# Optimization experiments

Measured on AMD Instinct MI355X. Metric: run time of the kernel, lower is better.

## Reference

```python
import jax, jax.numpy as jnp
import numpy as np

N_NODES = 4096
N_EDGES = 16384
L = 512
MP_STEPS = 5
DT = 0.01


def _mlp(x, W1, b1, W2, b2):
    return jax.nn.relu(x @ W1 + b1) @ W2 + b2


def _ln(x):
    m = jnp.mean(x, axis=-1, keepdims=True)
    v = jnp.var(x, axis=-1, keepdims=True)
    return (x - m) * jax.lax.rsqrt(v + 1e-6)


_PARAM_SHAPES = [
    ("enc_e_W1", (1, L)), ("enc_e_b1", (L,)), ("enc_e_W2", (L, L)), ("enc_e_b2", (L,)),
    ("enc_n_W1", (1, L)), ("enc_n_b1", (L,)), ("enc_n_W2", (L, L)), ("enc_n_b2", (L,)),
    ("proc_e_W1", (3 * L, L)), ("proc_e_b1", (L,)), ("proc_e_W2", (L, L)), ("proc_e_b2", (L,)),
    ("proc_n_W1", (2 * L, L)), ("proc_n_b1", (L,)), ("proc_n_W2", (L, L)), ("proc_n_b2", (L,)),
    ("dec_e_W1", (L, L)), ("dec_e_b1", (L,)), ("dec_e_W2", (L, 1)), ("dec_e_b2", (1,)),
]


def setup_inputs() -> dict:
    key = jax.random.key(0)
    ks = jax.random.split(key, 3 + len(_PARAM_SHAPES))
    d = {}
    d["state"] = jax.random.normal(ks[0], (N_EDGES + N_NODES,), dtype=jnp.float32)
    d["senders"] = jax.random.randint(ks[1], (N_EDGES,), 0, N_NODES)
    d["receivers"] = jax.random.randint(ks[2], (N_EDGES,), 0, N_NODES)
    for i, (name, shp) in enumerate(_PARAM_SHAPES):
        if name.endswith(("b1", "b2")):
            d[name] = jnp.zeros(shp, dtype=jnp.float32)
        else:
            d[name] = 0.02 * jax.random.normal(ks[3 + i], shp, dtype=jnp.float32)
    return d


def _hamiltonian(x, senders, receivers,
                 enc_e_W1, enc_e_b1, enc_e_W2, enc_e_b2,
                 enc_n_W1, enc_n_b1, enc_n_W2, enc_n_b2,
                 proc_e_W1, proc_e_b1, proc_e_W2, proc_e_b2,
                 proc_n_W1, proc_n_b1, proc_n_W2, proc_n_b2,
                 dec_e_W1, dec_e_b1, dec_e_W2, dec_e_b2):
    # graph_from_state: edge scalars then node scalars
    e = x[:N_EDGES].reshape(N_EDGES, 1)
    n = x[N_EDGES:].reshape(N_NODES, 1)
    # encode (MLP + layer norm)
    eh = _ln(_mlp(e, enc_e_W1, enc_e_b1, enc_e_W2, enc_e_b2))  # [E, L]
    nh = _ln(_mlp(n, enc_n_W1, enc_n_b1, enc_n_W2, enc_n_b2))  # [N, L]
    # process: num_mp_steps of GraphNetwork-style message passing, shared params
    for _ in range(MP_STEPS):
        msg_in = jnp.concatenate([eh, nh[senders], nh[receivers]], axis=-1)  # [E, 3L]
        eh = eh + _mlp(msg_in, proc_e_W1, proc_e_b1, proc_e_W2, proc_e_b2)
        agg = jax.ops.segment_sum(eh, receivers, num_segments=N_NODES)  # [N, L]
        node_in = jnp.concatenate([nh, agg], axis=-1)  # [N, 2L]
        nh = nh + _mlp(node_in, proc_n_W1, proc_n_b1, proc_n_W2, proc_n_b2)
    # decode edges to scalars; H = sum of decoded edge energies
    dec_e = _mlp(eh, dec_e_W1, dec_e_b1, dec_e_W2, dec_e_b2)  # [E, 1]
    return jnp.sum(dec_e)


def reference(state, senders, receivers,
              enc_e_W1, enc_e_b1, enc_e_W2, enc_e_b2,
              enc_n_W1, enc_n_b1, enc_n_W2, enc_n_b2,
              proc_e_W1, proc_e_b1, proc_e_W2, proc_e_b2,
              proc_n_W1, proc_n_b1, proc_n_W2, proc_n_b2,
              dec_e_W1, dec_e_b1, dec_e_W2, dec_e_b2):
    def H_fn(x):
        return _hamiltonian(x, senders, receivers,
                            enc_e_W1, enc_e_b1, enc_e_W2, enc_e_b2,
                            enc_n_W1, enc_n_b1, enc_n_W2, enc_n_b2,
                            proc_e_W1, proc_e_b1, proc_e_W2, proc_e_b2,
                            proc_n_W1, proc_n_b1, proc_n_W2, proc_n_b2,
                            dec_e_W1, dec_e_b1, dec_e_W2, dec_e_b2)
    H, dH = jax.value_and_grad(H_fn)(state)
    # one integrator step driven by the Hamiltonian gradient (stand-in for DAE solve)
    next_state = state - DT * dH
    return next_state
```

## Files before the change

kernel.cpp:

```cpp
#include <hip/hip_runtime.h>


#define E_ROWS 16384
#define N_ROWS 4096
#define DT_F   0.01f

typedef unsigned char u8;
typedef unsigned short u16;
typedef __attribute__((ext_vector_type(8))) short short8v;
typedef __attribute__((ext_vector_type(4))) float f32x4;

__device__ __forceinline__ u16 f2b(float f) {
    union { float f; unsigned u; } v; v.f = f;
    unsigned r = v.u + 0x7FFF + ((v.u >> 16) & 1);
    return (u16)(r >> 16);
}
__device__ __forceinline__ float b2f(u16 u) {
    union { unsigned u; float f; } v; v.u = ((unsigned)u) << 16;
    return v.f;
}

template<int KTOT, int LDA, int LDC, bool ADD_C, bool GATHER2, bool BIAS,
         bool RELU_MASK, bool APPLY_MASK, bool WF32, bool WBF16, bool DUALOUT>
__global__ __launch_bounds__(256)
void bgemm(const u16* __restrict__ A, const u16* __restrict__ Bt,
           float* __restrict__ C, u16* __restrict__ Cb,
           const float* __restrict__ Cin, const float* __restrict__ bias,
           const float* __restrict__ G12v,
           const int* __restrict__ sidx, const int* __restrict__ ridx,
           u8* __restrict__ maskw, float* __restrict__ C2)
{
    __shared__ u16 Al[4096];
    __shared__ u16 Bl[4096];
    const int tid = threadIdx.x;
    const int lane = tid & 63;
    const int wv = tid >> 6;
    const int wr = wv >> 1, wc = wv & 1;
    const int rowBase = blockIdx.y << 7;
    const int colBase = blockIdx.x << 7;

    const int srow = tid >> 2;
    const int kel = (tid & 3) << 3;
    const u16* Ag = A + (size_t)(rowBase + srow) * LDA + kel;
    const u16* Bg = Bt + (size_t)(colBase + srow) * KTOT + kel;
    u16* Ad = Al + (wv << 9);
    u16* Bd = Bl + (wv << 9);

    f32x4 acc[4][4];
#pragma unroll
    for (int i = 0; i < 4; ++i)
#pragma unroll
        for (int j = 0; j < 4; ++j)
            acc[i][j] = (f32x4){0.f, 0.f, 0.f, 0.f};

    const int arow = (wr << 6) + (lane & 15);
    const int brow = (wc << 6) + (lane & 15);
    const int koff = (lane >> 4) << 3;

    for (int kb = 0; kb < KTOT; kb += 32) {
        __builtin_amdgcn_global_load_lds((const __attribute__((address_space(1))) void*)(Ag + kb),
                                         (__attribute__((address_space(3))) void*)Ad, 16, 0, 0);
        __builtin_amdgcn_global_load_lds((const __attribute__((address_space(1))) void*)(Ag + kb + (size_t)64 * LDA),
                                         (__attribute__((address_space(3))) void*)(Ad + 2048), 16, 0, 0);
        __builtin_amdgcn_global_load_lds((const __attribute__((address_space(1))) void*)(Bg + kb),
                                         (__attribute__((address_space(3))) void*)Bd, 16, 0, 0);
        __builtin_amdgcn_global_load_lds((const __attribute__((address_space(1))) void*)(Bg + kb + (size_t)64 * KTOT),
                                         (__attribute__((address_space(3))) void*)(Bd + 2048), 16, 0, 0);
        __syncthreads();
        short8v af[4], bf[4];
#pragma unroll
        for (int i = 0; i < 4; ++i)
            af[i] = *(const short8v*)&Al[((arow + (i << 4)) << 5) + koff];
#pragma unroll
        for (int j = 0; j < 4; ++j)
            bf[j] = *(const short8v*)&Bl[((brow + (j << 4)) << 5) + koff];
#pragma unroll
        for (int i = 0; i < 4; ++i)
#pragma unroll
            for (int j = 0; j < 4; ++j)
                acc[i][j] = __builtin_amdgcn_mfma_f32_16x16x32_bf16(af[i], bf[j], acc[i][j], 0, 0, 0);
        __syncthreads();
    }

    const int colB = colBase + (wc << 6) + (lane & 15);
    const int rowB = rowBase + (wr << 6) + ((lane >> 4) << 2);
    float bcol[4];
    if (BIAS) {
#pragma unroll
        for (int j = 0; j < 4; ++j) bcol[j] = bias[colB + (j << 4)];
    }
    const bool upper = DUALOUT && (colBase >= 512);
#pragma unroll
    for (int i = 0; i < 4; ++i) {
#pragma unroll
        for (int r = 0; r < 4; ++r) {
            const int row = rowB + (i << 4) + r;
            int si = 0, ri = 0;
            if (GATHER2) { si = sidx[row]; ri = ridx[row]; }
#pragma unroll
            for (int j = 0; j < 4; ++j) {
                const int col = colB + (j << 4);
                float v = acc[i][j][r];
                if (DUALOUT) {
                    if (upper) {
                        C2[(size_t)row * 512 + (col - 512)] = v;
                    } else {
                        if (ADD_C) v += Cin[(size_t)row * 512 + col];
                        C[(size_t)row * 512 + col] = v;
                    }
                    continue;
                }
                if (GATHER2) v += G12v[(size_t)si * 1024 + col] + G12v[(size_t)ri * 1024 + 512 + col];
                if (ADD_C) v += Cin[(size_t)row * LDC + col];
                if (BIAS) v += bcol[j];
                const size_t o = (size_t)row * LDC + col;
                if (RELU_MASK) {
                    const u8 m = v > 0.f;
                    maskw[o] = m;
                    v = m ? v : 0.f;
                }
                if (APPLY_MASK) {
                    if (!maskw[o]) v = 0.f;
                }
                if (WF32) C[o] = v;
                if (WBF16) Cb[o] = f2b(v);
            }
        }
    }
}

struct WArgs {
    const float* src[10];
    u16* dstP[10];
    u16* dstT[10];
    int ldP[10], ldT[10];
};

__global__ void wcvt_kernel(WArgs a)
{
    const int i = blockIdx.z;
    const float* W = a.src[i];
    u16* P = a.dstP[i]; const int lp = a.ldP[i];
    u16* T = a.dstT[i]; const int lt = a.ldT[i];
    __shared__ u16 t[64][66];
    const int rb = blockIdx.y << 6, cb = blockIdx.x << 6;
    const int tr = threadIdx.x >> 4;
    const int tc = (threadIdx.x & 15) << 2;
#pragma unroll
    for (int rr = 0; rr < 4; ++rr) {
        const int r = tr + (rr << 4);
        const float4 v = *(const float4*)&W[(size_t)(rb + r) * 512 + cb + tc];
        ushort4 u; u.x = f2b(v.x); u.y = f2b(v.y); u.z = f2b(v.z); u.w = f2b(v.w);
        *(ushort4*)&P[(size_t)(rb + r) * lp + cb + tc] = u;
        t[r][tc] = u.x; t[r][tc + 1] = u.y; t[r][tc + 2] = u.z; t[r][tc + 3] = u.w;
    }
    __syncthreads();
#pragma unroll
    for (int rr = 0; rr < 4; ++rr) {
        const int n = tr + (rr << 4);
        ushort4 u;
        u.x = t[tc][n]; u.y = t[tc + 1][n]; u.z = t[tc + 2][n]; u.w = t[tc + 3][n];
        *(ushort4*)&T[(size_t)(cb + n) * lt + rb + tc] = u;
    }
}

__global__ __launch_bounds__(1024) void csr_build_kernel(const int* __restrict__ idx,
                                                         int* __restrict__ starts,
                                                         int* __restrict__ eids)
{
    __shared__ int hist[4096];
    __shared__ int scanbuf[1024];
    const int t = threadIdx.x;
    for (int i = t; i < 4096; i += 1024) hist[i] = 0;
    __syncthreads();
    for (int e = t; e < 16384; e += 1024) atomicAdd(&hist[idx[e]], 1);
    __syncthreads();
    const int base = t << 2;
    const int l0 = hist[base], l1 = hist[base + 1], l2 = hist[base + 2], l3 = hist[base + 3];
    const int lsum = l0 + l1 + l2 + l3;
    scanbuf[t] = lsum;
    __syncthreads();
    for (int ofs = 1; ofs < 1024; ofs <<= 1) {
        const int v = scanbuf[t];
        const int u = (t >= ofs) ? scanbuf[t - ofs] : 0;
        __syncthreads();
        scanbuf[t] = v + u;
        __syncthreads();
    }
    const int excl = scanbuf[t] - lsum;
    const int p0 = excl, p1 = p0 + l0, p2 = p1 + l1, p3 = p2 + l2;
    starts[base] = p0; starts[base + 1] = p1; starts[base + 2] = p2; starts[base + 3] = p3;
    if (t == 0) starts[4096] = 16384;
    __syncthreads();
    hist[base] = p0; hist[base + 1] = p1; hist[base + 2] = p2; hist[base + 3] = p3;
    __syncthreads();
    for (int e = t; e < 16384; e += 1024) {
        const int pos = atomicAdd(&hist[idx[e]], 1);
        eids[pos] = e;
    }
    __syncthreads();
    for (int n = t; n < 4096; n += 1024) {
        const int s0 = starts[n], s1 = hist[n];
        for (int i = s0 + 1; i < s1; ++i) {
            const int v = eids[i];
            int j = i - 1;
            while (j >= s0 && eids[j] > v) { eids[j + 1] = eids[j]; --j; }
            eids[j + 1] = v;
        }
    }
}

__global__ void seg_agg_fwd_kernel(const float* __restrict__ eh, const int* __restrict__ starts,
                                   const int* __restrict__ eids, const u16* __restrict__ nhb,
                                   u16* __restrict__ nagg)
{
    const int n = blockIdx.x, c = threadIdx.x;
    const int s0 = starts[n], s1 = starts[n + 1];
    float a0 = 0.f, a1 = 0.f;
    for (int i = s0; i < s1; ++i) {
        const float* p = eh + (size_t)eids[i] * 512;
        a0 += p[c]; a1 += p[c + 256];
    }
    u16* d = nagg + (size_t)n * 1024;
    const u16* s = nhb + (size_t)n * 512;
    d[c] = s[c]; d[c + 256] = s[c + 256];
    d[512 + c] = f2b(a0); d[768 + c] = f2b(a1);
}

__global__ void seg_sr_bwd_kernel(const u16* __restrict__ dh1e,
                                  const int* __restrict__ sst, const int* __restrict__ seid,
                                  const int* __restrict__ rst, const int* __restrict__ reid,
                                  u16* __restrict__ SR)
{
    const int n = blockIdx.x, c = threadIdx.x;
    float a0 = 0.f, a1 = 0.f, b0 = 0.f, b1 = 0.f;
    for (int i = sst[n]; i < sst[n + 1]; ++i) {
        const u16* p = dh1e + (size_t)seid[i] * 512;
        a0 += b2f(p[c]); a1 += b2f(p[c + 256]);
    }
    for (int i = rst[n]; i < rst[n + 1]; ++i) {
        const u16* p = dh1e + (size_t)reid[i] * 512;
        b0 += b2f(p[c]); b1 += b2f(p[c + 256]);
    }
    u16* d = SR + (size_t)n * 1024;
    d[c] = f2b(a0); d[c + 256] = f2b(a1);
    d[512 + c] = f2b(b0); d[768 + c] = f2b(b1);
}

__global__ void enc_h1_kernel(const float* __restrict__ x, const float* __restrict__ W1,
                              const float* __restrict__ b1, u16* __restrict__ h1b,
                              u8* __restrict__ mask)
{
    const int idx = blockIdx.x * 256 + threadIdx.x;
    const int row = idx >> 7;
    const int c = (idx & 127) << 2;
    const float xv = x[row];
    const float4 w = *(const float4*)&W1[c];
    const float4 b = *(const float4*)&b1[c];
    float4 v;
    v.x = fmaf(xv, w.x, b.x); v.y = fmaf(xv, w.y, b.y);
    v.z = fmaf(xv, w.z, b.z); v.w = fmaf(xv, w.w, b.w);
    uchar4 m;
    m.x = v.x > 0.f; m.y = v.y > 0.f; m.z = v.z > 0.f; m.w = v.w > 0.f;
    v.x = m.x ? v.x : 0.f; v.y = m.y ? v.y : 0.f;
    v.z = m.z ? v.z : 0.f; v.w = m.w ? v.w : 0.f;
    const size_t o = (size_t)row * 512 + c;
    ushort4 u; u.x = f2b(v.x); u.y = f2b(v.y); u.z = f2b(v.z); u.w = f2b(v.w);
    *(ushort4*)&h1b[o] = u;
    *(uchar4*)&mask[o] = m;
}

__global__ void ln_fwd_kernel(float* __restrict__ x, u16* __restrict__ xhat_b,
                              u16* __restrict__ xb, float* __restrict__ rstd_save)
{
    const int row = blockIdx.x, tid = threadIdx.x;
    float* p = x + (size_t)row * 512;
    const float a = p[tid], b = p[tid + 256];
    __shared__ float s1[256], s2[256];
    s1[tid] = a + b; s2[tid] = a * a + b * b;
    __syncthreads();
    for (int d = 128; d > 0; d >>= 1) {
        if (tid < d) { s1[tid] += s1[tid + d]; s2[tid] += s2[tid + d]; }
        __syncthreads();
    }
    const float mean = s1[0] * (1.f / 512.f);
    const float var = s2[0] * (1.f / 512.f) - mean * mean;
    const float r = rsqrtf(var + 1e-6f);
    const float ya = (a - mean) * r, yb = (b - mean) * r;
    p[tid] = ya; p[tid + 256] = yb;
    const size_t o = (size_t)row * 512 + tid;
    xhat_b[o] = f2b(ya); xhat_b[o + 256] = f2b(yb);
    xb[o] = f2b(ya); xb[o + 256] = f2b(yb);
    if (tid == 0) rstd_save[row] = r;
}

__global__ void ln_bwd_kernel(float* __restrict__ d, const u16* __restrict__ xhat_b,
                              const float* __restrict__ rstd, u16* __restrict__ db)
{
    const int row = blockIdx.x, tid = threadIdx.x;
    float* p = d + (size_t)row * 512;
    const u16* xh = xhat_b + (size_t)row * 512;
    const float da = p[tid], dbv = p[tid + 256];
    const float xa = b2f(xh[tid]), xbv = b2f(xh[tid + 256]);
    __shared__ float s1[256], s2[256];
    s1[tid] = da + dbv; s2[tid] = da * xa + dbv * xbv;
    __syncthreads();
    for (int dd = 128; dd > 0; dd >>= 1) {
        if (tid < dd) { s1[tid] += s1[tid + dd]; s2[tid] += s2[tid + dd]; }
        __syncthreads();
    }
    const float m1 = s1[0] * (1.f / 512.f);
    const float m2 = s2[0] * (1.f / 512.f);
    const float r = rstd[row];
    const float oa = r * (da - m1 - xa * m2);
    const float ob = r * (dbv - m1 - xbv * m2);
    p[tid] = oa; p[tid + 256] = ob;
    db[(size_t)row * 512 + tid] = f2b(oa);
    db[(size_t)row * 512 + tid + 256] = f2b(ob);
}

__global__ void gather_add_kernel(float* __restrict__ dst, u16* __restrict__ dstb,
                                  const float* __restrict__ src, const int* __restrict__ idx)
{
    const int t = blockIdx.x * 256 + threadIdx.x;
    const int row = t >> 7;
    const int c = (t & 127) << 2;
    const size_t o = (size_t)row * 512 + c;
    float4 a = *(const float4*)&dst[o];
    const float4 g = *(const float4*)&src[(size_t)idx[row] * 512 + c];
    a.x += g.x; a.y += g.y; a.z += g.z; a.w += g.w;
    *(float4*)&dst[o] = a;
    ushort4 u; u.x = f2b(a.x); u.y = f2b(a.y); u.z = f2b(a.z); u.w = f2b(a.w);
    *(ushort4*)&dstb[o] = u;
}

__global__ void dec_dh1_kernel(const u8* __restrict__ mask, const float* __restrict__ W2,
                               u16* __restrict__ dh1b)
{
    const int t = blockIdx.x * 256 + threadIdx.x;
    const int row = t >> 7;
    const int c = (t & 127) << 2;
    const size_t o = (size_t)row * 512 + c;
    const uchar4 m = *(const uchar4*)&mask[o];
    const float4 w = *(const float4*)&W2[c];
    ushort4 u;
    u.x = m.x ? f2b(w.x) : 0; u.y = m.y ? f2b(w.y) : 0;
    u.z = m.z ? f2b(w.z) : 0; u.w = m.w ? f2b(w.w) : 0;
    *(ushort4*)&dh1b[o] = u;
}

__global__ void rowdot_out_kernel(const u16* __restrict__ dh1b, const float* __restrict__ w,
                                  const float* __restrict__ xin, float* __restrict__ out)
{
    const int row = blockIdx.x, tid = threadIdx.x;
    const u16* p = dh1b + (size_t)row * 512;
    float s = b2f(p[tid]) * w[tid] + b2f(p[tid + 256]) * w[tid + 256];
    __shared__ float sh[256];
    sh[tid] = s;
    __syncthreads();
    for (int d = 128; d > 0; d >>= 1) {
        if (tid < d) sh[tid] += sh[tid + d];
        __syncthreads();
    }
    if (tid == 0) out[row] = xin[row] - DT_F * sh[0];
}

extern "C" void kernel_launch(void* const* d_in, const int* in_sizes, int n_in,
                              void* d_out, int out_size, void* d_ws, size_t ws_size,
                              hipStream_t stream)
{
    (void)in_sizes; (void)n_in; (void)out_size; (void)ws_size;
    const float* state     = (const float*)d_in[0];
    const int*   senders   = (const int*)d_in[1];
    const int*   receivers = (const int*)d_in[2];
    const float* enc_e_W1 = (const float*)d_in[3];
    const float* enc_e_b1 = (const float*)d_in[4];
    const float* enc_e_W2 = (const float*)d_in[5];
    const float* enc_e_b2 = (const float*)d_in[6];
    const float* enc_n_W1 = (const float*)d_in[7];
    const float* enc_n_b1 = (const float*)d_in[8];
    const float* enc_n_W2 = (const float*)d_in[9];
    const float* enc_n_b2 = (const float*)d_in[10];
    const float* pe_W1 = (const float*)d_in[11];
    const float* pe_b1 = (const float*)d_in[12];
    const float* pe_W2 = (const float*)d_in[13];
    const float* pe_b2 = (const float*)d_in[14];
    const float* pn_W1 = (const float*)d_in[15];
    const float* pn_b1 = (const float*)d_in[16];
    const float* pn_W2 = (const float*)d_in[17];
    const float* pn_b2 = (const float*)d_in[18];
    const float* de_W1 = (const float*)d_in[19];
    const float* de_b1 = (const float*)d_in[20];
    const float* de_W2 = (const float*)d_in[21];
    float* out = (float*)d_out;

    const size_t EL = (size_t)E_ROWS * 512, NL = (size_t)N_ROWS * 512;
    const size_t LL = 512 * 512;
    char* w = (char*)d_ws;
    size_t off = 0;
    auto carve = [&](size_t bytes) -> char* {
        char* p = w + off;
        off += (bytes + 255) & ~(size_t)255;
        return p;
    };
    u16* wb = (u16*)carve(20 * LL * 2);
    u16* WT0 = wb;           u16* WT1 = wb + LL;      u16* WT2 = wb + 2 * LL;
    u16* WT34 = wb + 3 * LL;    u16* WT5 = wb + 5 * LL;
    u16* WT8 = wb + 6 * LL;  u16* WT9 = wb + 7 * LL;
    u16* WP0 = wb + 8 * LL;  u16* WP1 = wb + 9 * LL;  u16* WP2 = wb + 10 * LL;
    u16* WP5 = wb + 11 * LL; u16* WP8 = wb + 12 * LL; u16* WP9 = wb + 13 * LL;
    u16* WT67 = wb + 14 * LL;
    u16* WP34c = wb + 16 * LL;
    u16* WP67 = wb + 18 * LL;

    float* eh  = (float*)carve(EL * 4);
    float* nh  = (float*)carve(NL * 4);
    float* G12 = (float*)carve(NL * 2 * 4);
    float* G1  = (float*)carve(NL * 4);
    u16* nsr   = (u16*)carve(NL * 2 * 2);
    u16* eh0b = (u16*)carve(EL * 2);
    u16* nh0b = (u16*)carve(NL * 2);
    u16* ehb  = (u16*)carve(EL * 2);
    u16* h1eb = (u16*)carve(EL * 2);
    u16* nhb  = (u16*)carve(NL * 2);
    u16* h1nb = (u16*)carve(NL * 2);
    float* rstd_e = (float*)carve(E_ROWS * 4);
    float* rstd_n = (float*)carve(N_ROWS * 4);
    u8* menc_e = (u8*)carve(EL);
    u8* menc_n = (u8*)carve(NL);
    u8* mpe    = (u8*)carve(5 * EL);
    u8* mpn    = (u8*)carve(5 * NL);
    u8* mdec   = (u8*)carve(EL);
    int* rst  = (int*)carve(4097 * 4);
    int* reid = (int*)carve(16384 * 4);
    int* sst  = (int*)carve(4097 * 4);
    int* seid = (int*)carve(16384 * 4);

    const dim3 blk(256);
    const dim3 gE(4, E_ROWS / 128), gN(4, N_ROWS / 128);
    const dim3 gN1024(8, N_ROWS / 128);
    const float* fp = nullptr;
    u16* up = nullptr;
    const int* ip = nullptr;
    u8* mp = nullptr;
    float* f2p = nullptr;

    WArgs wa;
    const float* wsrc[10] = { enc_e_W2, enc_n_W2, pe_W1, pe_W1 + LL, pe_W1 + 2 * LL,
                              pe_W2, pn_W1, pn_W1 + LL, pn_W2, de_W1 };
    u16* dstP[10] = { WP0, WP1, WP2, WP34c, WP34c + 512, WP5, WP67, WP67 + LL, WP8, WP9 };
    int  ldP [10] = { 512, 512, 512, 1024,  1024,        512, 512,  512,       512, 512 };
    u16* dstT[10] = { WT0, WT1, WT2, WT34, WT34 + LL, WT5, WT67, WT67 + 512, WT8, WT9 };
    int  ldT [10] = { 512, 512, 512, 512,  512,       512, 1024, 1024,       512, 512 };
    for (int i = 0; i < 10; ++i) {
        wa.src[i] = wsrc[i]; wa.dstP[i] = dstP[i]; wa.dstT[i] = dstT[i];
        wa.ldP[i] = ldP[i]; wa.ldT[i] = ldT[i];
    }
    wcvt_kernel<<<dim3(8, 8, 10), blk, 0, stream>>>(wa);

    csr_build_kernel<<<1, 1024, 0, stream>>>(receivers, rst, reid);
    csr_build_kernel<<<1, 1024, 0, stream>>>(senders, sst, seid);

    enc_h1_kernel<<<E_ROWS * 128 / 256, blk, 0, stream>>>(state, enc_e_W1, enc_e_b1, h1eb, menc_e);
    bgemm<512,512,512,false,false,true,false,false,true,false,false><<<gE, blk, 0, stream>>>(h1eb, WT0, eh, up, fp, enc_e_b2, fp, ip, ip, mp, f2p);
    ln_fwd_kernel<<<E_ROWS, blk, 0, stream>>>(eh, eh0b, ehb, rstd_e);
    enc_h1_kernel<<<N_ROWS * 128 / 256, blk, 0, stream>>>(state + E_ROWS, enc_n_W1, enc_n_b1, h1nb, menc_n);
    bgemm<512,512,512,false,false,true,false,false,true,false,false><<<gN, blk, 0, stream>>>(h1nb, WT1, nh, up, fp, enc_n_b2, fp, ip, ip, mp, f2p);
    ln_fwd_kernel<<<N_ROWS, blk, 0, stream>>>(nh, nh0b, nhb, rstd_n);

    for (int k = 0; k < 5; ++k) {
        bgemm<512,512,1024,false,false,false,false,false,true,false,false><<<gN1024, blk, 0, stream>>>(nhb, WT34, G12, up, fp, fp, fp, ip, ip, mp, f2p);
        bgemm<512,512,512,false,true,true,true,false,false,true,false><<<gE, blk, 0, stream>>>(ehb, WT2, nullptr, h1eb, fp, pe_b1, G12, senders, receivers, mpe + (size_t)k * EL, f2p);
        bgemm<512,512,512,true,false,true,false,false,true,true,false><<<gE, blk, 0, stream>>>(h1eb, WT5, eh, ehb, eh, pe_b2, fp, ip, ip, mp, f2p);
        seg_agg_fwd_kernel<<<N_ROWS, blk, 0, stream>>>(eh, rst, reid, nhb, nsr);
        bgemm<1024,1024,512,false,false,true,true,false,false,true,false><<<gN, blk, 0, stream>>>(nsr, WT67, nullptr, h1nb, fp, pn_b1, fp, ip, ip, mpn + (size_t)k * NL, f2p);
        bgemm<512,512,512,true,false,true,false,false,true,true,false><<<gN, blk, 0, stream>>>(h1nb, WT8, nh, nhb, nh, pn_b2, fp, ip, ip, mp, f2p);
    }

    bgemm<512,512,512,false,false,true,true,false,false,false,false><<<gE, blk, 0, stream>>>(ehb, WT9, nullptr, up, fp, de_b1, fp, ip, ip, mdec, f2p);

    dec_dh1_kernel<<<E_ROWS * 128 / 256, blk, 0, stream>>>(mdec, de_W2, h1eb);
    bgemm<512,512,512,false,false,false,false,false,true,true,false><<<gE, blk, 0, stream>>>(h1eb, WP9, eh, ehb, fp, fp, fp, ip, ip, mp, f2p);

    for (int k = 4; k >= 0; --k) {
        if (k < 4) {
            bgemm<512,512,512,false,false,false,false,true,false,true,false><<<gN, blk, 0, stream>>>(nhb, WP8, nullptr, h1nb, fp, fp, fp, ip, ip, mpn + (size_t)k * NL, f2p);
            bgemm<512,512,512,true,false,false,false,false,true,false,true><<<gN1024, blk, 0, stream>>>(h1nb, WP67, nh, up, nh, fp, fp, ip, ip, mp, G1);
            gather_add_kernel<<<E_ROWS * 128 / 256, blk, 0, stream>>>(eh, ehb, G1, receivers);
        }
        bgemm<512,512,512,false,false,false,false,true,false,true,false><<<gE, blk, 0, stream>>>(ehb, WP5, nullptr, h1eb, fp, fp, fp, ip, ip, mpe + (size_t)k * EL, f2p);
        bgemm<512,512,512,true,false,false,false,false,true,true,false><<<gE, blk, 0, stream>>>(h1eb, WP2, eh, ehb, eh, fp, fp, ip, ip, mp, f2p);
        seg_sr_bwd_kernel<<<N_ROWS, blk, 0, stream>>>(h1eb, sst, seid, rst, reid, nsr);
        if (k == 4)
            bgemm<1024,1024,512,false,false,false,false,false,true,true,false><<<gN, blk, 0, stream>>>(nsr, WP34c, nh, nhb, fp, fp, fp, ip, ip, mp, f2p);
        else
            bgemm<1024,1024,512,true,false,false,false,false,true,true,false><<<gN, blk, 0, stream>>>(nsr, WP34c, nh, nhb, nh, fp, fp, ip, ip, mp, f2p);
    }

    ln_bwd_kernel<<<E_ROWS, blk, 0, stream>>>(eh, eh0b, rstd_e, ehb);
    bgemm<512,512,512,false,false,false,false,true,false,true,false><<<gE, blk, 0, stream>>>(ehb, WP0, nullptr, h1eb, fp, fp, fp, ip, ip, menc_e, f2p);
    rowdot_out_kernel<<<E_ROWS, blk, 0, stream>>>(h1eb, enc_e_W1, state, out);
    ln_bwd_kernel<<<N_ROWS, blk, 0, stream>>>(nh, nh0b, rstd_n, nhb);
    bgemm<512,512,512,false,false,false,false,true,false,true,false><<<gN, blk, 0, stream>>>(nhb, WP1, nullptr, h1nb, fp, fp, fp, ip, ip, menc_n, f2p);
    rowdot_out_kernel<<<N_ROWS, blk, 0, stream>>>(h1nb, enc_n_W1, state + E_ROWS, out + E_ROWS);
}
```

Measured before the change: 1.478 ms.

## Retile GEMMs to 64-row blocks, fuse rowdot output, store gathers in bf16

Rewrites the bf16 MFMA GEMM so each block covers 64 rows, with a templated warp layout (1x4 or 2x2) and an XCD-aware block-index swizzle. This gives more blocks for the node-sized GEMMs and better L2 locality. The final row-dot output reduction is fused into the last backward GEMMs through shuffle reductions and atomics on an output buffer pre-initialised with the state. The G12 gather table and the edge aggregation input switch from fp32 to bf16 to cut memory traffic, and the two CSR builds are merged into one launch. The bf16 storage adds rounding error, and the atomic accumulation makes the sum order nondeterministic.

```diff
diff --git a/kernel.cpp b/kernel.cpp
--- a/kernel.cpp
+++ b/kernel.cpp
@@ -20,83 +20,99 @@
     return v.f;
 }
 
-template<int KTOT, int LDA, int LDC, bool ADD_C, bool GATHER2, bool BIAS,
-         bool RELU_MASK, bool APPLY_MASK, bool WF32, bool WBF16, bool DUALOUT>
+template<int WM, int WN, int KTOT, int LDA, int LDC,
+         bool ADD_C, bool GATHER2, bool BIAS, bool RELU_MASK, bool APPLY_MASK,
+         bool WF32, bool WBF16, bool DUALOUT, bool ROWDOT>
 __global__ __launch_bounds__(256)
 void bgemm(const u16* __restrict__ A, const u16* __restrict__ Bt,
            float* __restrict__ C, u16* __restrict__ Cb,
            const float* __restrict__ Cin, const float* __restrict__ bias,
-           const float* __restrict__ G12v,
+           const u16* __restrict__ G12b,
            const int* __restrict__ sidx, const int* __restrict__ ridx,
-           u8* __restrict__ maskw, float* __restrict__ C2)
-{
-    __shared__ u16 Al[4096];
-    __shared__ u16 Bl[4096];
+           u8* __restrict__ maskw, float* __restrict__ C2,
+           const float* __restrict__ w1f, float* __restrict__ outp)
+{
+    constexpr int BN = WN * 64;
+    constexpr int IFRAG = 4 / WM;
+    __shared__ u16 Al[2048];
+    __shared__ u16 Bl[512 * WN * 4];
+
     const int tid = threadIdx.x;
     const int lane = tid & 63;
     const int wv = tid >> 6;
-    const int wr = wv >> 1, wc = wv & 1;
-    const int rowBase = blockIdx.y << 7;
-    const int colBase = blockIdx.x << 7;
-
-    const int srow = tid >> 2;
-    const int kel = (tid & 3) << 3;
-    const u16* Ag = A + (size_t)(rowBase + srow) * LDA + kel;
-    const u16* Bg = Bt + (size_t)(colBase + srow) * KTOT + kel;
-    u16* Ad = Al + (wv << 9);
-    u16* Bd = Bl + (wv << 9);
-
-    f32x4 acc[4][4];
-#pragma unroll
-    for (int i = 0; i < 4; ++i)
+    const int wr = wv / WN;
+    const int wc = wv % WN;
+
+    const int gx = gridDim.x;
+    int id = blockIdx.y * gx + blockIdx.x;
+    const int nwg = gx * gridDim.y;
+    id = (id & 7) * (nwg >> 3) + (id >> 3);
+    const int bx = id % gx;
+    const int by = id / gx;
+
+    const int rowBase = by * 64;
+    const int colBase = bx * BN;
+
+    const int srow = lane & 15;
+    const int slotk = (lane >> 4) << 3;
+    const u16* Ag = A + (size_t)(rowBase + wv * 16 + srow) * LDA + slotk;
+
+    f32x4 acc[IFRAG][4];
+#pragma unroll
+    for (int i = 0; i < IFRAG; ++i)
 #pragma unroll
         for (int j = 0; j < 4; ++j)
             acc[i][j] = (f32x4){0.f, 0.f, 0.f, 0.f};
 
-    const int arow = (wr << 6) + (lane & 15);
-    const int brow = (wc << 6) + (lane & 15);
-    const int koff = (lane >> 4) << 3;
-
     for (int kb = 0; kb < KTOT; kb += 32) {
-        __builtin_amdgcn_global_load_lds((const __attribute__((address_space(1))) void*)(Ag + kb),
-                                         (__attribute__((address_space(3))) void*)Ad, 16, 0, 0);
-        __builtin_amdgcn_global_load_lds((const __attribute__((address_space(1))) void*)(Ag + kb + (size_t)64 * LDA),
-                                         (__attribute__((address_space(3))) void*)(Ad + 2048), 16, 0, 0);
-        __builtin_amdgcn_global_load_lds((const __attribute__((address_space(1))) void*)(Bg + kb),
-                                         (__attribute__((address_space(3))) void*)Bd, 16, 0, 0);
-        __builtin_amdgcn_global_load_lds((const __attribute__((address_space(1))) void*)(Bg + kb + (size_t)64 * KTOT),
-                                         (__attribute__((address_space(3))) void*)(Bd + 2048), 16, 0, 0);
+        __builtin_amdgcn_global_load_lds(
+            (const __attribute__((address_space(1))) void*)(Ag + kb),
+            (__attribute__((address_space(3))) void*)(Al + (wv << 9)), 16, 0, 0);
+#pragma unroll
+        for (int q = 0; q < WN; ++q) {
+            const int c = q * 4 + wv;
+            const u16* Bg = Bt + (size_t)(colBase + c * 16 + srow) * KTOT + kb + slotk;
+            __builtin_amdgcn_global_load_lds(
+                (const __attribute__((address_space(1))) void*)Bg,
+                (__attribute__((address_space(3))) void*)(Bl + (c << 9)), 16, 0, 0);
+        }
         __syncthreads();
-        short8v af[4], bf[4];
-#pragma unroll
-        for (int i = 0; i < 4; ++i)
-            af[i] = *(const short8v*)&Al[((arow + (i << 4)) << 5) + koff];
+        short8v af[IFRAG], bfm[4];
+        const int fro = ((lane >> 4) << 7) + ((lane & 15) << 3);
+#pragma unroll
+        for (int i = 0; i < IFRAG; ++i)
+            af[i] = *(const short8v*)&Al[((wr * IFRAG + i) << 9) + fro];
 #pragma unroll
         for (int j = 0; j < 4; ++j)
-            bf[j] = *(const short8v*)&Bl[((brow + (j << 4)) << 5) + koff];
-#pragma unroll
-        for (int i = 0; i < 4; ++i)
+            bfm[j] = *(const short8v*)&Bl[((wc * 4 + j) << 9) + fro];
+#pragma unroll
+        for (int i = 0; i < IFRAG; ++i)
 #pragma unroll
             for (int j = 0; j < 4; ++j)
-                acc[i][j] = __builtin_amdgcn_mfma_f32_16x16x32_bf16(af[i], bf[j], acc[i][j], 0, 0, 0);
+                acc[i][j] = __builtin_amdgcn_mfma_f32_16x16x32_bf16(af[i], bfm[j], acc[i][j], 0, 0, 0);
         __syncthreads();
     }
 
-    const int colB = colBase + (wc << 6) + (lane & 15);
-    const int rowB = rowBase + (wr << 6) + ((lane >> 4) << 2);
-    float bcol[4];
+    const int colB = colBase + wc * 64 + (lane & 15);
+    const int rowB = rowBase + wr * (IFRAG * 16) + ((lane >> 4) << 2);
+    float bcol[4], w1c[4];
     if (BIAS) {
 #pragma unroll
         for (int j = 0; j < 4; ++j) bcol[j] = bias[colB + (j << 4)];
     }
+    if (ROWDOT) {
+#pragma unroll
+        for (int j = 0; j < 4; ++j) w1c[j] = w1f[colB + (j << 4)];
+    }
     const bool upper = DUALOUT && (colBase >= 512);
 #pragma unroll
-    for (int i = 0; i < 4; ++i) {
+    for (int i = 0; i < IFRAG; ++i) {
 #pragma unroll
         for (int r = 0; r < 4; ++r) {
             const int row = rowB + (i << 4) + r;
             int si = 0, ri = 0;
             if (GATHER2) { si = sidx[row]; ri = ridx[row]; }
+            float rds = 0.f;
 #pragma unroll
             for (int j = 0; j < 4; ++j) {
                 const int col = colB + (j << 4);
@@ -110,20 +126,26 @@
                     }
                     continue;
                 }
-                if (GATHER2) v += G12v[(size_t)si * 1024 + col] + G12v[(size_t)ri * 1024 + 512 + col];
+                if (GATHER2) v += b2f(G12b[(size_t)si * 1024 + col]) + b2f(G12b[(size_t)ri * 1024 + 512 + col]);
                 if (ADD_C) v += Cin[(size_t)row * LDC + col];
                 if (BIAS) v += bcol[j];
-                const size_t o = (size_t)row * LDC + col;
                 if (RELU_MASK) {
                     const u8 m = v > 0.f;
-                    maskw[o] = m;
+                    maskw[(size_t)row * 512 + col] = m;
                     v = m ? v : 0.f;
                 }
                 if (APPLY_MASK) {
-                    if (!maskw[o]) v = 0.f;
+                    if (!maskw[(size_t)row * 512 + col]) v = 0.f;
                 }
+                if (ROWDOT) rds += v * w1c[j];
+                const size_t o = (size_t)row * LDC + col;
                 if (WF32) C[o] = v;
                 if (WBF16) Cb[o] = f2b(v);
+            }
+            if (ROWDOT) {
+#pragma unroll
+                for (int m = 1; m < 16; m <<= 1) rds += __shfl_xor(rds, m);
+                if ((lane & 15) == 0) atomicAdd(outp + row, -DT_F * rds);
             }
         }
     }
@@ -164,9 +186,8 @@
     }
 }
 
-__global__ __launch_bounds__(1024) void csr_build_kernel(const int* __restrict__ idx,
-                                                         int* __restrict__ starts,
-                                                         int* __restrict__ eids)
+__device__ void csr_build(const int* __restrict__ idx, int* __restrict__ starts,
+                          int* __restrict__ eids)
 {
     __shared__ int hist[4096];
     __shared__ int scanbuf[1024];
@@ -210,7 +231,22 @@
     }
 }
 
-__global__ void seg_agg_fwd_kernel(const float* __restrict__ eh, const int* __restrict__ starts,
+__global__ __launch_bounds__(1024) void csr2_kernel(const int* __restrict__ senders,
+                                                    const int* __restrict__ receivers,
+                                                    int* __restrict__ sst, int* __restrict__ seid,
+                                                    int* __restrict__ rst, int* __restrict__ reid)
+{
+    if (blockIdx.x == 0) csr_build(receivers, rst, reid);
+    else                 csr_build(senders, sst, seid);
+}
+
+__global__ void init_out_kernel(const float* __restrict__ state, float* __restrict__ out)
+{
+    const int t = blockIdx.x * 256 + threadIdx.x;
+    out[t] = state[t];
+}
+
+__global__ void seg_agg_fwd_kernel(const u16* __restrict__ ehb, const int* __restrict__ starts,
                                    const int* __restrict__ eids, const u16* __restrict__ nhb,
                                    u16* __restrict__ nagg)
 {
@@ -218,8 +254,8 @@
     const int s0 = starts[n], s1 = starts[n + 1];
     float a0 = 0.f, a1 = 0.f;
     for (int i = s0; i < s1; ++i) {
-        const float* p = eh + (size_t)eids[i] * 512;
-        a0 += p[c]; a1 += p[c + 256];
+        const u16* p = ehb + (size_t)eids[i] * 512;
+        a0 += b2f(p[c]); a1 += b2f(p[c + 256]);
     }
     u16* d = nagg + (size_t)n * 1024;
     const u16* s = nhb + (size_t)n * 512;
@@ -347,22 +383,6 @@
     u.x = m.x ? f2b(w.x) : 0; u.y = m.y ? f2b(w.y) : 0;
     u.z = m.z ? f2b(w.z) : 0; u.w = m.w ? f2b(w.w) : 0;
     *(ushort4*)&dh1b[o] = u;
-}
-
-__global__ void rowdot_out_kernel(const u16* __restrict__ dh1b, const float* __restrict__ w,
-                                  const float* __restrict__ xin, float* __restrict__ out)
-{
-    const int row = blockIdx.x, tid = threadIdx.x;
-    const u16* p = dh1b + (size_t)row * 512;
-    float s = b2f(p[tid]) * w[tid] + b2f(p[tid + 256]) * w[tid + 256];
-    __shared__ float sh[256];
-    sh[tid] = s;
-    __syncthreads();
-    for (int d = 128; d > 0; d >>= 1) {
-        if (tid < d) sh[tid] += sh[tid + d];
-        __syncthreads();
-    }
-    if (tid == 0) out[row] = xin[row] - DT_F * sh[0];
 }
 
 extern "C" void kernel_launch(void* const* d_in, const int* in_sizes, int n_in,
@@ -405,7 +425,7 @@
     };
     u16* wb = (u16*)carve(20 * LL * 2);
     u16* WT0 = wb;           u16* WT1 = wb + LL;      u16* WT2 = wb + 2 * LL;
-    u16* WT34 = wb + 3 * LL;    u16* WT5 = wb + 5 * LL;
+    u16* WT34 = wb + 3 * LL;                          u16* WT5 = wb + 5 * LL;
     u16* WT8 = wb + 6 * LL;  u16* WT9 = wb + 7 * LL;
     u16* WP0 = wb + 8 * LL;  u16* WP1 = wb + 9 * LL;  u16* WP2 = wb + 10 * LL;
     u16* WP5 = wb + 11 * LL; u16* WP8 = wb + 12 * LL; u16* WP9 = wb + 13 * LL;
@@ -415,8 +435,8 @@
 
     float* eh  = (float*)carve(EL * 4);
     float* nh  = (float*)carve(NL * 4);
-    float* G12 = (float*)carve(NL * 2 * 4);
     float* G1  = (float*)carve(NL * 4);
+    u16* G12b  = (u16*)carve(NL * 2 * 2);
     u16* nsr   = (u16*)carve(NL * 2 * 2);
     u16* eh0b = (u16*)carve(EL * 2);
     u16* nh0b = (u16*)carve(NL * 2);
@@ -437,10 +457,12 @@
     int* seid = (int*)carve(16384 * 4);
 
     const dim3 blk(256);
-    const dim3 gE(4, E_ROWS / 128), gN(4, N_ROWS / 128);
-    const dim3 gN1024(8, N_ROWS / 128);
+    const dim3 gE(2, E_ROWS / 64);
+    const dim3 gN(4, N_ROWS / 64);
+    const dim3 gN1024(4, N_ROWS / 64);
     const float* fp = nullptr;
     u16* up = nullptr;
+    const u16* cup = nullptr;
     const int* ip = nullptr;
     u8* mp = nullptr;
     float* f2p = nullptr;
@@ -458,49 +480,64 @@
     }
     wcvt_kernel<<<dim3(8, 8, 10), blk, 0, stream>>>(wa);
 
-    csr_build_kernel<<<1, 1024, 0, stream>>>(receivers, rst, reid);
-    csr_build_kernel<<<1, 1024, 0, stream>>>(senders, sst, seid);
+    csr2_kernel<<<2, 1024, 0, stream>>>(senders, receivers, sst, seid, rst, reid);
+    init_out_kernel<<<(E_ROWS + N_ROWS) / 256, blk, 0, stream>>>(state, out);
 
     enc_h1_kernel<<<E_ROWS * 128 / 256, blk, 0, stream>>>(state, enc_e_W1, enc_e_b1, h1eb, menc_e);
-    bgemm<512,512,512,false,false,true,false,false,true,false,false><<<gE, blk, 0, stream>>>(h1eb, WT0, eh, up, fp, enc_e_b2, fp, ip, ip, mp, f2p);
+    bgemm<1,4,512,512,512, false,false,true,false,false, true,false,false,false>
+        <<<gE, blk, 0, stream>>>(h1eb, WT0, eh, up, fp, enc_e_b2, cup, ip, ip, mp, f2p, fp, f2p);
     ln_fwd_kernel<<<E_ROWS, blk, 0, stream>>>(eh, eh0b, ehb, rstd_e);
     enc_h1_kernel<<<N_ROWS * 128 / 256, blk, 0, stream>>>(state + E_ROWS, enc_n_W1, enc_n_b1, h1nb, menc_n);
-    bgemm<512,512,512,false,false,true,false,false,true,false,false><<<gN, blk, 0, stream>>>(h1nb, WT1, nh, up, fp, enc_n_b2, fp, ip, ip, mp, f2p);
+    bgemm<2,2,512,512,512, false,false,true,false,false, true,false,false,false>
+        <<<gN, blk, 0, stream>>>(h1nb, WT1, nh, up, fp, enc_n_b2, cup, ip, ip, mp, f2p, fp, f2p);
     ln_fwd_kernel<<<N_ROWS, blk, 0, stream>>>(nh, nh0b, nhb, rstd_n);
 
     for (int k = 0; k < 5; ++k) {
-        bgemm<512,512,1024,false,false,false,false,false,true,false,false><<<gN1024, blk, 0, stream>>>(nhb, WT34, G12, up, fp, fp, fp, ip, ip, mp, f2p);
-        bgemm<512,512,512,false,true,true,true,false,false,true,false><<<gE, blk, 0, stream>>>(ehb, WT2, nullptr, h1eb, fp, pe_b1, G12, senders, receivers, mpe + (size_t)k * EL, f2p);
-        bgemm<512,512,512,true,false,true,false,false,true,true,false><<<gE, blk, 0, stream>>>(h1eb, WT5, eh, ehb, eh, pe_b2, fp, ip, ip, mp, f2p);
-        seg_agg_fwd_kernel<<<N_ROWS, blk, 0, stream>>>(eh, rst, reid, nhb, nsr);
-        bgemm<1024,1024,512,false,false,true,true,false,false,true,false><<<gN, blk, 0, stream>>>(nsr, WT67, nullptr, h1nb, fp, pn_b1, fp, ip, ip, mpn + (size_t)k * NL, f2p);
-        bgemm<512,512,512,true,false,true,false,false,true,true,false><<<gN, blk, 0, stream>>>(h1nb, WT8, nh, nhb, nh, pn_b2, fp, ip, ip, mp, f2p);
-    }
-
-    bgemm<512,512,512,false,false,true,true,false,false,false,false><<<gE, blk, 0, stream>>>(ehb, WT9, nullptr, up, fp, de_b1, fp, ip, ip, mdec, f2p);
+        bgemm<1,4,512,512,1024, false,false,false,false,false, false,true,false,false>
+            <<<gN1024, blk, 0, stream>>>(nhb, WT34, f2p, G12b, fp, fp, cup, ip, ip, mp, f2p, fp, f2p);
+        bgemm<1,4,512,512,512, false,true,true,true,false, false,true,false,false>
+            <<<gE, blk, 0, stream>>>(ehb, WT2, f2p, h1eb, fp, pe_b1, G12b, senders, receivers, mpe + (size_t)k * EL, f2p, fp, f2p);
+        bgemm<1,4,512,512,512, true,false,true,false,false, true,true,false,false>
+            <<<gE, blk, 0, stream>>>(h1eb, WT5, eh, ehb, eh, pe_b2, cup, ip, ip, mp, f2p, fp, f2p);
+        seg_agg_fwd_kernel<<<N_ROWS, blk, 0, stream>>>(ehb, rst, reid, nhb, nsr);
+        bgemm<2,2,1024,1024,512, false,false,true,true,false, false,true,false,false>
+            <<<gN, blk, 0, stream>>>(nsr, WT67, f2p, h1nb, fp, pn_b1, cup, ip, ip, mpn + (size_t)k * NL, f2p, fp, f2p);
+        bgemm<2,2,512,512,512, true,false,true,false,false, true,true,false,false>
+            <<<gN, blk, 0, stream>>>(h1nb, WT8, nh, nhb, nh, pn_b2, cup, ip, ip, mp, f2p, fp, f2p);
+    }
+
+    bgemm<1,4,512,512,512, false,false,true,true,false, false,false,false,false>
+        <<<gE, blk, 0, stream>>>(ehb, WT9, f2p, up, fp, de_b1, cup, ip, ip, mdec, f2p, fp, f2p);
 
     dec_dh1_kernel<<<E_ROWS * 128 / 256, blk, 0, stream>>>(mdec, de_W2, h1eb);
-    bgemm<512,512,512,false,false,false,false,false,true,true,false><<<gE, blk, 0, stream>>>(h1eb, WP9, eh, ehb, fp, fp, fp, ip, ip, mp, f2p);
+    bgemm<1,4,512,512,512, false,false,false,false,false, true,true,false,false>
+        <<<gE, blk, 0, stream>>>(h1eb, WP9, eh, ehb, fp, fp, cup, ip, ip, mp, f2p, fp, f2p);
 
     for (int k = 4; k >= 0; --k) {
         if (k < 4) {
-            bgemm<512,512,512,false,false,false,false,true,false,true,false><<<gN, blk, 0, stream>>>(nhb, WP8, nullptr, h1nb, fp, fp, fp, ip, ip, mpn + (size_t)k * NL, f2p);
-            bgemm<512,512,512,true,false,false,false,false,true,false,true><<<gN1024, blk, 0, stream>>>(h1nb, WP67, nh, up, nh, fp, fp, ip, ip, mp, G1);
+            bgemm<2,2,512,512,512, false,false,false,false,true, false,true,false,false>
+                <<<gN, blk, 0, stream>>>(nhb, WP8, f2p, h1nb, fp, fp, cup, ip, ip, mpn + (size_t)k * NL, f2p, fp, f2p);
+            bgemm<1,4,512,512,512, true,false,false,false,false, true,false,true,false>
+                <<<gN1024, blk, 0, stream>>>(h1nb, WP67, nh, up, nh, fp, cup, ip, ip, mp, G1, fp, f2p);
             gather_add_kernel<<<E_ROWS * 128 / 256, blk, 0, stream>>>(eh, ehb, G1, receivers);
         }
-        bgemm<512,512,512,false,false,false,false,true,false,true,false><<<gE, blk, 0, stream>>>(ehb, WP5, nullptr, h1eb, fp, fp, fp, ip, ip, mpe + (size_t)k * EL, f2p);
-        bgemm<512,512,512,true,false,false,false,false,true,true,false><<<gE, blk, 0, stream>>>(h1eb, WP2, eh, ehb, eh, fp, fp, ip, ip, mp, f2p);
+        bgemm<1,4,512,512,512, false,false,false,false,true, false,true,false,false>
+            <<<gE, blk, 0, stream>>>(ehb, WP5, f2p, h1eb, fp, fp, cup, ip, ip, mpe + (size_t)k * EL, f2p, fp, f2p);
+        bgemm<1,4,512,512,512, true,false,false,false,false, true,true,false,false>
+            <<<gE, blk, 0, stream>>>(h1eb, WP2, eh, ehb, eh, fp, cup, ip, ip, mp, f2p, fp, f2p);
         seg_sr_bwd_kernel<<<N_ROWS, blk, 0, stream>>>(h1eb, sst, seid, rst, reid, nsr);
         if (k == 4)
-            bgemm<1024,1024,512,false,false,false,false,false,true,true,false><<<gN, blk, 0, stream>>>(nsr, WP34c, nh, nhb, fp, fp, fp, ip, ip, mp, f2p);
+            bgemm<2,2,1024,1024,512, false,false,false,false,false, true,true,false,false>
+                <<<gN, blk, 0, stream>>>(nsr, WP34c, nh, nhb, fp, fp, cup, ip, ip, mp, f2p, fp, f2p);
         else
-            bgemm<1024,1024,512,true,false,false,false,false,true,true,false><<<gN, blk, 0, stream>>>(nsr, WP34c, nh, nhb, nh, fp, fp, ip, ip, mp, f2p);
+            bgemm<2,2,1024,1024,512, true,false,false,false,false, true,true,false,false>
+                <<<gN, blk, 0, stream>>>(nsr, WP34c, nh, nhb, nh, fp, cup, ip, ip, mp, f2p, fp, f2p);
     }
 
     ln_bwd_kernel<<<E_ROWS, blk, 0, stream>>>(eh, eh0b, rstd_e, ehb);
-    bgemm<512,512,512,false,false,false,false,true,false,true,false><<<gE, blk, 0, stream>>>(ehb, WP0, nullptr, h1eb, fp, fp, fp, ip, ip, menc_e, f2p);
-    rowdot_out_kernel<<<E_ROWS, blk, 0, stream>>>(h1eb, enc_e_W1, state, out);
+    bgemm<1,4,512,512,512, false,false,false,false,true, false,false,false,true>
+        <<<gE, blk, 0, stream>>>(ehb, WP0, f2p, up, fp, fp, cup, ip, ip, menc_e, f2p, enc_e_W1, out);
     ln_bwd_kernel<<<N_ROWS, blk, 0, stream>>>(nh, nh0b, rstd_n, nhb);
-    bgemm<512,512,512,false,false,false,false,true,false,true,false><<<gN, blk, 0, stream>>>(nhb, WP1, nullptr, h1nb, fp, fp, fp, ip, ip, menc_n, f2p);
-    rowdot_out_kernel<<<N_ROWS, blk, 0, stream>>>(h1nb, enc_n_W1, state + E_ROWS, out + E_ROWS);
-}
+    bgemm<2,2,512,512,512, false,false,false,false,true, false,false,false,true>
+        <<<gN, blk, 0, stream>>>(nhb, WP1, f2p, up, fp, fp, cup, ip, ip, menc_n, f2p, enc_n_W1, out + E_ROWS);
+}
```

After: 1.634 ms. 1.11x slower.
